# Performance work log

Measured on AMD Instinct MI355X. Metric: run time of the kernel, lower is better.

## Reference

```python
import jax, jax.numpy as jnp
import numpy as np

H, P, T = 256, 16, 4      # hidden_size, maxout_pool_size, max_dec_steps
B, M = 32, 600            # batch, document length

def _lstm_cell(x, h, c, W_ih, W_hh, b_ih, b_hh):
    g = x @ W_ih.T + b_ih + h @ W_hh.T + b_hh
    i, f, gg, o = jnp.split(g, 4, axis=1)  # torch gate order i,f,g,o
    c = jax.nn.sigmoid(f) * c + jax.nn.sigmoid(i) * jnp.tanh(gg)
    h = jax.nn.sigmoid(o) * jnp.tanh(c)
    return h, c

def _maxout(h, U, u_cat, mask_mult, W_lin, W1, b1, W2, b2, W12, b12):
    b, m, _ = U.shape
    r = jnp.tanh(jnp.concatenate([h, u_cat], axis=1) @ W_lin.T)                  # [b,H]
    m1_in = jnp.concatenate([U, jnp.broadcast_to(r[:, None, :], (b, m, H))], 2)  # [b,m,3H]
    m1 = (m1_in @ W1.T + b1).reshape(b, m, H, P).max(-1)                         # [b,m,H]
    m2 = (m1 @ W2.T + b2).reshape(b, m, H, P).max(-1)                            # [b,m,H]
    alpha = (jnp.concatenate([m1, m2], axis=2) @ W12.T + b12).max(-1)            # [b,m]
    return jax.nn.log_softmax(alpha + mask_mult, axis=1)

def _forward(U, d_mask, span, W_ih, W_hh, b_ih, b_hh,
             Ws_lin, Ws_m1, bs_m1, Ws_m2, bs_m2, Ws_m12, bs_m12,
             We_lin, We_m1, be_m1, We_m2, be_m2, We_m12, be_m12):
    b, m, _ = U.shape
    idxb = jnp.arange(b)
    mask_mult = (1.0 - d_mask.astype(U.dtype)) * -1e30
    s_i = jnp.zeros(b, jnp.int32)
    e_i = (jnp.sum(d_mask, 1) - 1).astype(jnp.int32)
    s_tgt, e_tgt = span[:, 0], span[:, 1]
    h = jnp.zeros((b, H), U.dtype)
    c = jnp.zeros((b, H), U.dtype)
    mask_s = mask_e = None
    res_s, res_e, res_ms, res_me, losses = [], [], [], [], []
    u_s = U[idxb, s_i]
    for t in range(T):
        u_e = U[idxb, e_i]
        u_cat = jnp.concatenate([u_s, u_e], axis=1)
        h, c = _lstm_cell(u_cat, h, c, W_ih, W_hh, b_ih, b_hh)
        # start pointer
        lsm = _maxout(h, U, u_cat, mask_mult, Ws_lin, Ws_m1, bs_m1, Ws_m2, bs_m2, Ws_m12, bs_m12)
        idx = jnp.argmax(lsm, axis=1).astype(jnp.int32)
        if t == 0:
            mask_s = jnp.ones(b, bool)
        else:
            idx = idx * mask_s.astype(jnp.int32)
            prev = s_i * mask_s.astype(jnp.int32)
            mask_s = idx != prev
        loss_s = jnp.mean(-jnp.take_along_axis(lsm, s_tgt[:, None], 1)[:, 0]) * mask_s.astype(U.dtype)
        s_i = idx
        u_s = U[idxb, s_i]
        # end pointer
        u_cat2 = jnp.concatenate([u_s, u_e], axis=1)
        lsm_e = _maxout(h, U, u_cat2, mask_mult, We_lin, We_m1, be_m1, We_m2, be_m2, We_m12, be_m12)
        idx_e = jnp.argmax(lsm_e, axis=1).astype(jnp.int32)
        if t == 0:
            mask_e = jnp.ones(b, bool)
        else:
            idx_e = idx_e * mask_e.astype(jnp.int32)
            prev_e = e_i * mask_e.astype(jnp.int32)
            mask_e = idx_e != prev_e
        loss_e = jnp.mean(-jnp.take_along_axis(lsm_e, e_tgt[:, None], 1)[:, 0]) * mask_e.astype(U.dtype)
        e_i = idx_e
        losses.append(loss_s + loss_e)
        res_s.append(s_i); res_ms.append(mask_s)
        res_e.append(e_i); res_me.append(mask_e)
    pos_s = jnp.sum(jnp.stack(res_ms, 1).astype(jnp.int32), 1) - 1
    p1 = jnp.take_along_axis(jnp.stack(res_s, 1), pos_s[:, None], 1)[:, 0]
    pos_e = jnp.sum(jnp.stack(res_me, 1).astype(jnp.int32), 1) - 1
    p2 = jnp.take_along_axis(jnp.stack(res_e, 1), pos_e[:, None], 1)[:, 0]
    loss = jnp.mean(jnp.sum(jnp.stack(losses, 1), 1) / T)
    return loss, p1, p2

def setup_inputs():
    key = jax.random.key(0)
    ks = jax.random.split(key, 16)
    U = jax.random.normal(ks[0], (B, M, 2 * H), jnp.float32)
    lengths = jax.random.randint(ks[1], (B,), M // 2, M + 1)
    d_mask = (jnp.arange(M)[None, :] < lengths[:, None]).astype(jnp.int32)
    span = jax.random.randint(ks[2], (B, 2), 0, M // 2).astype(jnp.int32)
    def w(k, shape, fan_in):
        return (jax.random.normal(k, shape, jnp.float32) / np.float32(np.sqrt(fan_in)))
    b_ih = jnp.zeros(4 * H, jnp.float32).at[H:2 * H].set(1.0)  # forget-gate bias init
    params = {
        'W_ih': w(ks[3], (4 * H, 4 * H), 4 * H), 'W_hh': w(ks[4], (4 * H, H), H),
        'b_ih': b_ih, 'b_hh': jnp.zeros(4 * H, jnp.float32),
        'Ws_lin': w(ks[5], (H, 5 * H), 5 * H),
        'Ws_m1': w(ks[6], (H * P, 3 * H), 3 * H), 'bs_m1': jnp.zeros(H * P, jnp.float32),
        'Ws_m2': w(ks[7], (H * P, H), H), 'bs_m2': jnp.zeros(H * P, jnp.float32),
        'Ws_m12': w(ks[8], (P, 2 * H), 2 * H), 'bs_m12': jnp.zeros(P, jnp.float32),
        'We_lin': w(ks[9], (H, 5 * H), 5 * H),
        'We_m1': w(ks[10], (H * P, 3 * H), 3 * H), 'be_m1': jnp.zeros(H * P, jnp.float32),
        'We_m2': w(ks[11], (H * P, H), H), 'be_m2': jnp.zeros(H * P, jnp.float32),
        'We_m12': w(ks[12], (P, 2 * H), 2 * H), 'be_m12': jnp.zeros(P, jnp.float32),
    }
    return {'U': U, 'd_mask': d_mask, 'span': span, **params}

def reference(U, d_mask, span, W_ih, W_hh, b_ih, b_hh,
              Ws_lin, Ws_m1, bs_m1, Ws_m2, bs_m2, Ws_m12, bs_m12,
              We_lin, We_m1, be_m1, We_m2, be_m2, We_m12, be_m12):
    return _forward(U, d_mask, span, W_ih, W_hh, b_ih, b_hh,
                    Ws_lin, Ws_m1, bs_m1, Ws_m2, bs_m2, Ws_m12, bs_m12,
                    We_lin, We_m1, be_m1, We_m2, be_m2, We_m12, be_m12)
```

## Files before the change

kernel.cpp:

```cpp
#include <hip/hip_runtime.h>
#include <math.h>

namespace {

typedef unsigned short u16;
typedef __attribute__((ext_vector_type(4))) float f32x4;
typedef __attribute__((ext_vector_type(8))) _Float16 f16x8;
typedef __attribute__((ext_vector_type(4))) _Float16 f16x4;

constexpr int B = 32;
constexpr int M = 600;
constexpr int H = 256;
constexpr int TSTEPS = 4;
constexpr int HP = 4096;
constexpr int BM = B * M;
constexpr int TWOH = 512;
constexpr int THREEH = 768;
constexpr int FOURH = 1024;
constexpr int FIVEH = 1280;
constexpr int NTILES = BM / 128;

__device__ __forceinline__ float sigf(float x) { return 1.0f / (1.0f + expf(-x)); }

__device__ __forceinline__ void gload16(const u16* g, u16* l) {
    __builtin_amdgcn_global_load_lds(
        (const __attribute__((address_space(1))) void*)g,
        (__attribute__((address_space(3))) void*)l, 16, 0, 0);
}

__global__ void k_init(const int* __restrict__ d_mask,
                       float* __restrict__ h, float* __restrict__ c,
                       float* __restrict__ loss_vec,
                       int* __restrict__ s_i, int* __restrict__ e_i,
                       int* __restrict__ p1r, int* __restrict__ p2r)
{
    int tid = threadIdx.x;
    for (int i = tid; i < B * H; i += 256) { h[i] = 0.f; c[i] = 0.f; }
    if (tid < B) {
        loss_vec[tid] = 0.f;
        s_i[tid] = 0;
        int s = 0;
        const int* row = d_mask + tid * M;
        for (int m = 0; m < M; ++m) s += row[m];
        e_i[tid] = s - 1;
        p1r[tid] = 0; p2r[tid] = 0;
    }
}

__global__ __launch_bounds__(128) void k_flags(const int* __restrict__ d_mask,
                                               int* __restrict__ flags)
{
    int bm = blockIdx.x * 128 + threadIdx.x;
    int cnt = __syncthreads_count(d_mask[bm]);
    if (threadIdx.x == 0) flags[blockIdx.x] = (cnt == 0) ? 1 : 0;
}

__global__ __launch_bounds__(256) void k_gather(
    const float* __restrict__ U, const int* __restrict__ s_i,
    const int* __restrict__ e_i, float* __restrict__ u_cat)
{
    int idx = blockIdx.x * 256 + threadIdx.x;
    int b = idx >> 9, k = idx & 511;
    u_cat[b * FOURH + k]       = U[((size_t)b * M + s_i[b]) * TWOH + k];
    u_cat[b * FOURH + 512 + k] = U[((size_t)b * M + e_i[b]) * TWOH + k];
}

__global__ __launch_bounds__(256) void k_lstm_gemm2(
    const float* __restrict__ U, const int* __restrict__ s_i,
    const int* __restrict__ e_i, const float* __restrict__ h,
    const float* __restrict__ W_ih, const float* __restrict__ W_hh,
    const float* __restrict__ b_ih, const float* __restrict__ b_hh,
    float* __restrict__ g)
{
    int idx = blockIdx.x * 256 + threadIdx.x;
    int b = idx >> 10, j = idx & 1023;
    const float* us = U + ((size_t)b * M + s_i[b]) * TWOH;
    const float* ue = U + ((size_t)b * M + e_i[b]) * TWOH;
    float acc = 0.f;
    const float4* x4 = (const float4*)us;
    const float4* wi4 = (const float4*)(W_ih + (size_t)j * FOURH);
    #pragma unroll 4
    for (int k = 0; k < TWOH / 4; ++k) {
        float4 a = x4[k], w = wi4[k];
        acc += a.x * w.x + a.y * w.y + a.z * w.z + a.w * w.w;
    }
    const float4* y4 = (const float4*)ue;
    const float4* wi4b = wi4 + TWOH / 4;
    #pragma unroll 4
    for (int k = 0; k < TWOH / 4; ++k) {
        float4 a = y4[k], w = wi4b[k];
        acc += a.x * w.x + a.y * w.y + a.z * w.z + a.w * w.w;
    }
    const float4* h4 = (const float4*)(h + b * H);
    const float4* wh4 = (const float4*)(W_hh + (size_t)j * H);
    #pragma unroll 4
    for (int k = 0; k < H / 4; ++k) {
        float4 a = h4[k], w = wh4[k];
        acc += a.x * w.x + a.y * w.y + a.z * w.z + a.w * w.w;
    }
    g[idx] = acc + b_ih[j] + b_hh[j];
}

__global__ __launch_bounds__(256) void k_lstm_gemm(
    const float* __restrict__ u_cat, const float* __restrict__ h,
    const float* __restrict__ W_ih, const float* __restrict__ W_hh,
    const float* __restrict__ b_ih, const float* __restrict__ b_hh,
    float* __restrict__ g)
{
    int idx = blockIdx.x * 256 + threadIdx.x;
    int b = idx >> 10, j = idx & 1023;
    float acc = 0.f;
    const float4* x4 = (const float4*)(u_cat + b * FOURH);
    const float4* wi4 = (const float4*)(W_ih + (size_t)j * FOURH);
    #pragma unroll 4
    for (int k = 0; k < FOURH / 4; ++k) {
        float4 a = x4[k], w = wi4[k];
        acc += a.x * w.x + a.y * w.y + a.z * w.z + a.w * w.w;
    }
    const float4* h4 = (const float4*)(h + b * H);
    const float4* wh4 = (const float4*)(W_hh + (size_t)j * H);
    #pragma unroll 4
    for (int k = 0; k < H / 4; ++k) {
        float4 a = h4[k], w = wh4[k];
        acc += a.x * w.x + a.y * w.y + a.z * w.z + a.w * w.w;
    }
    g[idx] = acc + b_ih[j] + b_hh[j];
}

__global__ __launch_bounds__(256) void k_lstm_gates(
    const float* __restrict__ g, float* __restrict__ h, float* __restrict__ c)
{
    int idx = blockIdx.x * 256 + threadIdx.x;
    int b = idx >> 8, i = idx & (H - 1);
    const float* gr = g + b * FOURH;
    float gi = gr[i], gf = gr[H + i], gg = gr[2 * H + i], go = gr[3 * H + i];
    float cn = sigf(gf) * c[idx] + sigf(gi) * tanhf(gg);
    c[idx] = cn;
    h[idx] = sigf(go) * tanhf(cn);
}

__global__ __launch_bounds__(256) void k_r2(
    const float* __restrict__ h, const float* __restrict__ U,
    const int* __restrict__ s_i, const int* __restrict__ e_i,
    const float* __restrict__ W_lin, float* __restrict__ r)
{
    int gid = blockIdx.x * 256 + threadIdx.x;
    int out = gid >> 2;
    int part = gid & 3;
    int b = out >> 8, i = out & (H - 1);
    const float4* w4 = (const float4*)(W_lin + (size_t)i * FIVEH);
    const float4* h4 = (const float4*)(h + b * H);
    const float4* us4 = (const float4*)(U + ((size_t)b * M + s_i[b]) * TWOH);
    const float4* ue4 = (const float4*)(U + ((size_t)b * M + e_i[b]) * TWOH);
    float acc = 0.f;
    int k0 = part * 80;
    #pragma unroll 4
    for (int kk = k0; kk < k0 + 80; ++kk) {
        float4 a;
        if (kk < 64) a = h4[kk];
        else if (kk < 192) a = us4[kk - 64];
        else a = ue4[kk - 192];
        float4 ww = w4[kk];
        acc += a.x * ww.x + a.y * ww.y + a.z * ww.z + a.w * ww.w;
    }
    acc += __shfl_xor(acc, 1);
    acc += __shfl_xor(acc, 2);
    if (part == 0) r[out] = tanhf(acc);
}

__global__ __launch_bounds__(256) void k_r(
    const float* __restrict__ h, const float* __restrict__ u_cat,
    const float* __restrict__ W_lin, float* __restrict__ r)
{
    int idx = blockIdx.x * 256 + threadIdx.x;
    int b = idx >> 8, i = idx & (H - 1);
    const float* w = W_lin + (size_t)i * FIVEH;
    float acc = 0.f;
    const float4* h4 = (const float4*)(h + b * H);
    const float4* w4 = (const float4*)w;
    #pragma unroll 4
    for (int k = 0; k < H / 4; ++k) {
        float4 a = h4[k], ww = w4[k];
        acc += a.x * ww.x + a.y * ww.y + a.z * ww.z + a.w * ww.w;
    }
    const float4* x4 = (const float4*)(u_cat + b * FOURH);
    const float4* w4b = (const float4*)(w + H);
    #pragma unroll 4
    for (int k = 0; k < FOURH / 4; ++k) {
        float4 a = x4[k], ww = w4b[k];
        acc += a.x * ww.x + a.y * ww.y + a.z * ww.z + a.w * ww.w;
    }
    r[idx] = tanhf(acc);
}

__global__ __launch_bounds__(256) void k_rW(
    const float* __restrict__ r, const float* __restrict__ W1,
    const float* __restrict__ b1, float* __restrict__ rW)
{
    int idx = blockIdx.x * 256 + threadIdx.x;
    int b = idx >> 12, j = idx & (HP - 1);
    const float4* r4 = (const float4*)(r + b * H);
    const float4* w4 = (const float4*)(W1 + (size_t)j * THREEH + TWOH);
    float acc = 0.f;
    #pragma unroll 4
    for (int k = 0; k < H / 4; ++k) {
        float4 a = r4[k], w = w4[k];
        acc += a.x * w.x + a.y * w.y + a.z * w.z + a.w * w.w;
    }
    rW[idx] = acc + b1[j];
}

__global__ __launch_bounds__(256) void k_rW2(
    const float* __restrict__ r, const float* __restrict__ Wt,
    const float* __restrict__ b1, float* __restrict__ rW)
{
    const int b = blockIdx.y;
    const int j = blockIdx.x * 256 + threadIdx.x;
    __shared__ float sr[256];
    sr[threadIdx.x] = r[b * H + threadIdx.x];
    __syncthreads();
    float acc = b1[j];
    #pragma unroll 4
    for (int k = 0; k < H; ++k) acc += sr[k] * Wt[(size_t)k * HP + j];
    rW[(size_t)b * HP + j] = acc;
}

__global__ __launch_bounds__(256) void k_transp2(
    const float* __restrict__ W, float* __restrict__ Wt)
{
    __shared__ float s[32][33];
    int j0 = (blockIdx.x & 127) << 5;
    int k0 = (blockIdx.x >> 7) << 5;
    int tx = threadIdx.x & 31, ty = threadIdx.x >> 5;
    #pragma unroll
    for (int kk = 0; kk < 4; ++kk) {
        int jl = ty + kk * 8;
        s[jl][tx] = W[(size_t)(j0 + jl) * THREEH + TWOH + k0 + tx];
    }
    __syncthreads();
    #pragma unroll
    for (int kk = 0; kk < 4; ++kk) {
        int kl = ty + kk * 8;
        Wt[(size_t)(k0 + kl) * HP + j0 + tx] = s[tx][kl];
    }
}

__global__ __launch_bounds__(256) void k_cvtH(
    const float* __restrict__ src, int ld, int Kc, _Float16* __restrict__ dst)
{
    int i4 = blockIdx.x * 256 + threadIdx.x;
    int perrow = Kc >> 2;
    int row = i4 / perrow;
    int kc = (i4 - row * perrow) << 2;
    float4 v = *(const float4*)(src + (size_t)row * ld + kc);
    f16x4 o;
    o[0] = (_Float16)v.x; o[1] = (_Float16)v.y; o[2] = (_Float16)v.z; o[3] = (_Float16)v.w;
    *(f16x4*)(dst + (size_t)row * Kc + kc) = o;
}

template <int EPI>
__global__ __launch_bounds__(256, 4) void gemmJ(
    const _Float16* __restrict__ A, const _Float16* __restrict__ Bw,
    int K, const float* __restrict__ extra, const int* __restrict__ skip,
    float* __restrict__ Cf, _Float16* __restrict__ Ch)
{
    if (skip[blockIdx.y]) return;
    __shared__ __align__(16) u16 sA[2][128 * 32];
    __shared__ __align__(16) u16 sB[2][128 * 32];
    const int tid = threadIdx.x;
    const int w = tid >> 6, lane = tid & 63;
    const int row0 = blockIdx.y * 128, col0 = blockIdx.x * 128;
    const int wm = w & 1, wn = w >> 1;

    const int r1g = tid >> 2,        k1 = (tid & 3) ^ ((r1g >> 1) & 3);
    const int r2g = (tid + 256) >> 2, k2 = ((tid + 256) & 3) ^ ((r2g >> 1) & 3);
    const size_t gA1 = (size_t)(row0 + r1g) * K + k1 * 8;
    const size_t gA2 = (size_t)(row0 + r2g) * K + k2 * 8;
    const size_t gB1 = (size_t)(col0 + r1g) * K + k1 * 8;
    const size_t gB2 = (size_t)(col0 + r2g) * K + k2 * 8;

    f32x4 acc[4][4] = {};

    gload16((const u16*)(A  + gA1), &sA[0][tid * 8]);
    gload16((const u16*)(A  + gA2), &sA[0][(tid + 256) * 8]);
    gload16((const u16*)(Bw + gB1), &sB[0][tid * 8]);
    gload16((const u16*)(Bw + gB2), &sB[0][(tid + 256) * 8]);

    const int iters = K >> 5;
    const int mrow = lane & 15;
    const int kg = lane >> 4;
    const int slot = kg ^ ((mrow >> 1) & 3);
    const int eoff = slot << 3;

    for (int it = 0; it < iters; ++it) {
        const int cur = it & 1;
        __syncthreads();
        if (it + 1 < iters) {
            const int k0n = (it + 1) << 5;
            gload16((const u16*)(A  + gA1 + k0n), &sA[1 - cur][tid * 8]);
            gload16((const u16*)(A  + gA2 + k0n), &sA[1 - cur][(tid + 256) * 8]);
            gload16((const u16*)(Bw + gB1 + k0n), &sB[1 - cur][tid * 8]);
            gload16((const u16*)(Bw + gB2 + k0n), &sB[1 - cur][(tid + 256) * 8]);
        }
        const u16* pa = &sA[cur][(wm * 64 + mrow) * 32 + eoff];
        const u16* pb = &sB[cur][(wn * 64 + mrow) * 32 + eoff];
        f16x8 fa[4], fb[4];
        #pragma unroll
        for (int f = 0; f < 4; ++f) {
            fa[f] = *(const f16x8*)(pa + f * 16 * 32);
            fb[f] = *(const f16x8*)(pb + f * 16 * 32);
        }
        #pragma unroll
        for (int i = 0; i < 4; ++i) {
            #pragma unroll
            for (int j = 0; j < 4; ++j) {
                acc[i][j] = __builtin_amdgcn_mfma_f32_16x16x32_f16(fa[i], fb[j], acc[i][j], 0, 0, 0);
            }
        }
    }

    const int cq = lane & 15, rq = lane >> 4;
    if (EPI == 4) {
        #pragma unroll
        for (int i = 0; i < 4; ++i) {
            #pragma unroll
            for (int j = 0; j < 4; ++j) {
                int col = col0 + wn * 64 + j * 16 + cq;
                #pragma unroll
                for (int rr = 0; rr < 4; ++rr) {
                    int row = row0 + wm * 64 + i * 16 + rq * 4 + rr;
                    Ch[(size_t)row * HP + col] = (_Float16)acc[i][j][rr];
                }
            }
        }
    } else if (EPI == 1) {
        #pragma unroll
        for (int j = 0; j < 4; ++j) {
            int col = col0 + wn * 64 + j * 16 + cq;
            int gcol = (col0 >> 4) + wn * 4 + j;
            float bv = extra[col];
            #pragma unroll
            for (int i = 0; i < 4; ++i) {
                #pragma unroll
                for (int rr = 0; rr < 4; ++rr) {
                    float v = acc[i][j][rr] + bv;
                    v = fmaxf(v, __shfl_xor(v, 1));
                    v = fmaxf(v, __shfl_xor(v, 2));
                    v = fmaxf(v, __shfl_xor(v, 4));
                    v = fmaxf(v, __shfl_xor(v, 8));
                    if (cq == 0) {
                        int row = row0 + wm * 64 + i * 16 + rq * 4 + rr;
                        Ch[(size_t)row * H + gcol] = (_Float16)v;
                    }
                }
            }
        }
    } else {
        const int rbase = row0 + wm * 64;
        const int b0 = rbase / M;
        const int bnd = (b0 + 1) * M;
        #pragma unroll
        for (int j = 0; j < 4; ++j) {
            int col = col0 + wn * 64 + j * 16 + cq;
            int gcol = (col0 >> 4) + wn * 4 + j;
            float e0 = extra[(size_t)b0 * HP + col];
            float e1 = extra[(size_t)(b0 + 1) * HP + col];
            #pragma unroll
            for (int i = 0; i < 4; ++i) {
                #pragma unroll
                for (int rr = 0; rr < 4; ++rr) {
                    int row = rbase + i * 16 + rq * 4 + rr;
                    float v = acc[i][j][rr] + ((row >= bnd) ? e1 : e0);
                    v = fmaxf(v, __shfl_xor(v, 1));
                    v = fmaxf(v, __shfl_xor(v, 2));
                    v = fmaxf(v, __shfl_xor(v, 4));
                    v = fmaxf(v, __shfl_xor(v, 8));
                    if (cq == 0)
                        Ch[(size_t)row * H + gcol] = (_Float16)v;
                }
            }
        }
    }
}

__global__ __launch_bounds__(256) void k_m1A16(
    const _Float16* __restrict__ A, const float* __restrict__ rW,
    _Float16* __restrict__ m1)
{
    int idx = blockIdx.x * 256 + threadIdx.x;
    int bm = idx >> 8;
    int h = idx & (H - 1);
    int b = bm / M;
    const f16x8* a8 = (const f16x8*)(A + (size_t)bm * HP + (h << 4));
    const float4* r4 = (const float4*)(rW + (size_t)b * HP + (h << 4));
    f16x8 a0 = a8[0], a1 = a8[1];
    float4 ra = r4[0], rb = r4[1], rc = r4[2], rd = r4[3];
    float mx;
    mx = fmaxf(fmaxf(fmaxf((float)a0[0] + ra.x, (float)a0[1] + ra.y),
                     fmaxf((float)a0[2] + ra.z, (float)a0[3] + ra.w)),
         fmaxf(fmaxf((float)a0[4] + rb.x, (float)a0[5] + rb.y),
               fmaxf((float)a0[6] + rb.z, (float)a0[7] + rb.w)));
    mx = fmaxf(mx,
         fmaxf(fmaxf(fmaxf((float)a1[0] + rc.x, (float)a1[1] + rc.y),
                     fmaxf((float)a1[2] + rc.z, (float)a1[3] + rc.w)),
               fmaxf(fmaxf((float)a1[4] + rd.x, (float)a1[5] + rd.y),
                     fmaxf((float)a1[6] + rd.z, (float)a1[7] + rd.w))));
    m1[idx] = (_Float16)mx;
}

template <int EPI>
__global__ __launch_bounds__(256) void gemm64(
    const float* __restrict__ Ag, int lda,
    const float* __restrict__ Bg, int ldb,
    const float* __restrict__ extra,
    float* __restrict__ C, int K, int ldc)
{
    __shared__ float As[16][68];
    __shared__ float Bs[16][68];
    const int tid = threadIdx.x;
    const int tx = tid & 15;
    const int ty = tid >> 4;
    const int row0 = blockIdx.y * 64;
    const int col0 = blockIdx.x * 64;
    const int lr = tid >> 2;
    const int lk = (tid & 3) << 2;
    const float* Aload = Ag + (size_t)(row0 + lr) * lda + lk;
    const float* Bload = Bg + (size_t)(col0 + lr) * ldb + lk;
    float acc[4][4] = {};
    for (int k0 = 0; k0 < K; k0 += 16) {
        float4 av = *(const float4*)(Aload + k0);
        float4 bv = *(const float4*)(Bload + k0);
        __syncthreads();
        As[lk + 0][lr] = av.x; As[lk + 1][lr] = av.y; As[lk + 2][lr] = av.z; As[lk + 3][lr] = av.w;
        Bs[lk + 0][lr] = bv.x; Bs[lk + 1][lr] = bv.y; Bs[lk + 2][lr] = bv.z; Bs[lk + 3][lr] = bv.w;
        __syncthreads();
        #pragma unroll
        for (int k = 0; k < 16; ++k) {
            float4 a4 = *(const float4*)(&As[k][ty << 2]);
            float4 b4 = *(const float4*)(&Bs[k][tx << 2]);
            acc[0][0] += a4.x * b4.x; acc[0][1] += a4.x * b4.y; acc[0][2] += a4.x * b4.z; acc[0][3] += a4.x * b4.w;
            acc[1][0] += a4.y * b4.x; acc[1][1] += a4.y * b4.y; acc[1][2] += a4.y * b4.z; acc[1][3] += a4.y * b4.w;
            acc[2][0] += a4.z * b4.x; acc[2][1] += a4.z * b4.y; acc[2][2] += a4.z * b4.z; acc[2][3] += a4.z * b4.w;
            acc[3][0] += a4.w * b4.x; acc[3][1] += a4.w * b4.y; acc[3][2] += a4.w * b4.z; acc[3][3] += a4.w * b4.w;
        }
    }
    if (EPI == 1) {
        const int cb = col0 + (tx << 2);
        float b0 = extra[cb], b1v = extra[cb + 1], b2v = extra[cb + 2], b3v = extra[cb + 3];
        #pragma unroll
        for (int i = 0; i < 4; ++i) {
            float mth = fmaxf(fmaxf(acc[i][0] + b0, acc[i][1] + b1v),
                              fmaxf(acc[i][2] + b2v, acc[i][3] + b3v));
            float r1 = fmaxf(mth, __shfl_xor(mth, 1));
            float r2 = fmaxf(r1, __shfl_xor(r1, 2));
            if ((tx & 3) == 0)
                C[(size_t)(row0 + (ty << 2) + i) * ldc + (col0 >> 4) + (tx >> 2)] = r2;
        }
    } else if (EPI == 2) {
        const int cb = col0 + (tx << 2);
        #pragma unroll
        for (int i = 0; i < 4; ++i) {
            int row = row0 + (ty << 2) + i;
            int b = row / M;
            const float* rw = extra + (size_t)b * HP + cb;
            float mth = fmaxf(fmaxf(acc[i][0] + rw[0], acc[i][1] + rw[1]),
                              fmaxf(acc[i][2] + rw[2], acc[i][3] + rw[3]));
            float r1 = fmaxf(mth, __shfl_xor(mth, 1));
            float r2 = fmaxf(r1, __shfl_xor(r1, 2));
            if ((tx & 3) == 0)
                C[(size_t)row * ldc + (col0 >> 4) + (tx >> 2)] = r2;
        }
    }
}

__global__ __launch_bounds__(256) void k_alpha(
    const float* __restrict__ m1, const float* __restrict__ m2,
    const float* __restrict__ W12, const float* __restrict__ b12,
    const int* __restrict__ d_mask, float* __restrict__ alpha)
{
    __shared__ float Ws[16 * 512];
    const int tid = threadIdx.x;
    for (int i = tid; i < 16 * 512; i += 256) Ws[i] = W12[i];
    __syncthreads();
    const int wave = tid >> 6, lane = tid & 63;
    const int bm = blockIdx.x * 4 + wave;
    const float* r1 = m1 + (size_t)bm * H;
    const float* r2 = m2 + (size_t)bm * H;
    float acc[16] = {};
    #pragma unroll
    for (int q = 0; q < 4; ++q) {
        int k = lane + (q << 6);
        float x = r1[k];
        #pragma unroll
        for (int p = 0; p < 16; ++p) acc[p] += x * Ws[p * 512 + k];
    }
    #pragma unroll
    for (int q = 0; q < 4; ++q) {
        int k = lane + (q << 6);
        float x = r2[k];
        #pragma unroll
        for (int p = 0; p < 16; ++p) acc[p] += x * Ws[p * 512 + 256 + k];
    }
    #pragma unroll
    for (int p = 0; p < 16; ++p) {
        float v = acc[p];
        v += __shfl_xor(v, 1);  v += __shfl_xor(v, 2);  v += __shfl_xor(v, 4);
        v += __shfl_xor(v, 8);  v += __shfl_xor(v, 16); v += __shfl_xor(v, 32);
        acc[p] = v;
    }
    if (lane == 0) {
        float mx = -INFINITY;
        #pragma unroll
        for (int p = 0; p < 16; ++p) mx = fmaxf(mx, acc[p] + b12[p]);
        alpha[bm] = d_mask[bm] ? mx : -1e30f;
    }
}

__global__ __launch_bounds__(256) void k_alpha2(
    const _Float16* __restrict__ m1, const _Float16* __restrict__ m2,
    const float* __restrict__ W12, const float* __restrict__ b12,
    const int* __restrict__ d_mask, float* __restrict__ alpha)
{
    __shared__ float Ws[16 * 512];
    const int tid = threadIdx.x;
    for (int i = tid; i < 16 * 512; i += 256) Ws[i] = W12[i];
    __syncthreads();
    const int wave = tid >> 6, lane = tid & 63;
    const int bm0 = blockIdx.x * 16 + wave * 4;
    for (int rr = 0; rr < 4; ++rr) {
        const int bm = bm0 + rr;
        if (!d_mask[bm]) {
            if (lane == 0) alpha[bm] = -1e30f;
            continue;
        }
        const _Float16* r1 = m1 + (size_t)bm * H;
        const _Float16* r2 = m2 + (size_t)bm * H;
        float acc[16] = {};
        #pragma unroll
        for (int q = 0; q < 4; ++q) {
            int k = lane + (q << 6);
            float x = (float)r1[k];
            #pragma unroll
            for (int p = 0; p < 16; ++p) acc[p] += x * Ws[p * 512 + k];
        }
        #pragma unroll
        for (int q = 0; q < 4; ++q) {
            int k = lane + (q << 6);
            float x = (float)r2[k];
            #pragma unroll
            for (int p = 0; p < 16; ++p) acc[p] += x * Ws[p * 512 + 256 + k];
        }
        #pragma unroll
        for (int p = 0; p < 16; ++p) {
            float v = acc[p];
            v += __shfl_xor(v, 1);  v += __shfl_xor(v, 2);  v += __shfl_xor(v, 4);
            v += __shfl_xor(v, 8);  v += __shfl_xor(v, 16); v += __shfl_xor(v, 32);
            acc[p] = v;
        }
        if (lane == 0) {
            float mx = -INFINITY;
            #pragma unroll
            for (int p = 0; p < 16; ++p) mx = fmaxf(mx, acc[p] + b12[p]);
            alpha[bm] = mx;
        }
    }
}

__global__ __launch_bounds__(1024) void k_smu(
    const float* __restrict__ alpha, const int* __restrict__ span, int phase,
    int* __restrict__ pos, int* __restrict__ mask,
    int* __restrict__ prun, float* __restrict__ loss_vec, int t)
{
    __shared__ float s_loss[B];
    __shared__ int s_idx[B];
    const int wave = threadIdx.x >> 6, lane = threadIdx.x & 63;
    for (int b = wave; b < B; b += 16) {
        const float* row = alpha + b * M;
        float best = -INFINITY; int bidx = 0;
        for (int m = lane; m < M; m += 64) {
            float v = row[m];
            if (v > best) { best = v; bidx = m; }
        }
        #pragma unroll
        for (int off = 1; off < 64; off <<= 1) {
            float v2 = __shfl_xor(best, off);
            int i2 = __shfl_xor(bidx, off);
            if (v2 > best || (v2 == best && i2 < bidx)) { best = v2; bidx = i2; }
        }
        float ps = 0.f;
        for (int m = lane; m < M; m += 64) ps += expf(row[m] - best);
        #pragma unroll
        for (int off = 32; off > 0; off >>= 1) ps += __shfl_xor(ps, off);
        if (lane == 0) {
            float lse = best + logf(ps);
            int tgt = span[b * 2 + phase];
            s_loss[b] = -(row[tgt] - lse);
            s_idx[b] = bidx;
        }
    }
    __syncthreads();
    if (wave == 0) {
        int b = lane;
        int active = (b < B) ? 1 : 0;
        int ni = 0, nm = 0;
        if (active) {
            int id = s_idx[b];
            if (t == 0) { nm = 1; ni = id; }
            else {
                int om = mask[b];
                ni = id * om;
                int prev = pos[b] * om;
                nm = (ni != prev) ? 1 : 0;
            }
        }
        float v = active ? s_loss[b] : 0.f;
        #pragma unroll
        for (int off = 32; off > 0; off >>= 1) v += __shfl_xor(v, off);
        float S = v * (1.0f / (float)B);
        if (active) {
            pos[b] = ni;
            mask[b] = nm;
            if (nm) { prun[b] = ni; loss_vec[b] += S; }
        }
    }
}

__global__ __launch_bounds__(256) void k_softmax(
    const float* __restrict__ alpha, const int* __restrict__ span, int phase,
    float* __restrict__ loss_term, int* __restrict__ idx_out)
{
    __shared__ float sv[256];
    __shared__ int si[256];
    const int b = blockIdx.x, tid = threadIdx.x;
    const float* row = alpha + b * M;
    float best = -INFINITY; int bidx = 0;
    for (int m = tid; m < M; m += 256) {
        float v = row[m];
        if (v > best) { best = v; bidx = m; }
    }
    sv[tid] = best; si[tid] = bidx;
    __syncthreads();
    for (int s = 128; s > 0; s >>= 1) {
        if (tid < s) {
            float v2 = sv[tid + s]; int i2 = si[tid + s];
            if (v2 > sv[tid] || (v2 == sv[tid] && i2 < si[tid])) { sv[tid] = v2; si[tid] = i2; }
        }
        __syncthreads();
    }
    float bmax = sv[0]; int amax = si[0];
    __syncthreads();
    float ps = 0.f;
    for (int m = tid; m < M; m += 256) ps += expf(row[m] - bmax);
    sv[tid] = ps;
    __syncthreads();
    for (int s = 128; s > 0; s >>= 1) {
        if (tid < s) sv[tid] += sv[tid + s];
        __syncthreads();
    }
    if (tid == 0) {
        float lse = bmax + logf(sv[0]);
        int tgt = span[b * 2 + phase];
        loss_term[b] = -(row[tgt] - lse);
        idx_out[b] = amax;
    }
}

__global__ void k_update(const int* __restrict__ idx_in, const float* __restrict__ loss_term,
                         int* __restrict__ pos, int* __restrict__ mask,
                         int* __restrict__ prun, float* __restrict__ loss_vec, int t)
{
    int b = threadIdx.x;
    int active = (b < B) ? 1 : 0;
    int ni = 0, nm = 0;
    if (active) {
        int id = idx_in[b];
        if (t == 0) { nm = 1; ni = id; }
        else {
            int om = mask[b];
            ni = id * om;
            int prev = pos[b] * om;
            nm = (ni != prev) ? 1 : 0;
        }
    }
    float v = active ? loss_term[b] : 0.f;
    #pragma unroll
    for (int off = 32; off > 0; off >>= 1) v += __shfl_xor(v, off);
    float S = v * (1.0f / (float)B);
    if (active) {
        pos[b] = ni;
        mask[b] = nm;
        if (nm) { prun[b] = ni; loss_vec[b] += S; }
    }
}

__global__ void k_finalize(const float* __restrict__ loss_vec, const int* __restrict__ p1r,
                           const int* __restrict__ p2r, float* __restrict__ out)
{
    int b = threadIdx.x;
    float v = (b < B) ? loss_vec[b] : 0.f;
    #pragma unroll
    for (int off = 32; off > 0; off >>= 1) v += __shfl_xor(v, off);
    if (b == 0) out[0] = v / (float)(B * TSTEPS);
    if (b < B) {
        out[1 + b] = (float)p1r[b];
        out[1 + B + b] = (float)p2r[b];
    }
}

}

extern "C" void kernel_launch(void* const* d_in, const int* in_sizes, int n_in,
                              void* d_out, int out_size, void* d_ws, size_t ws_size,
                              hipStream_t stream)
{
    const float* U      = (const float*)d_in[0];
    const int*   d_mask = (const int*)d_in[1];
    const int*   span   = (const int*)d_in[2];
    const float* W_ih   = (const float*)d_in[3];
    const float* W_hh   = (const float*)d_in[4];
    const float* b_ih   = (const float*)d_in[5];
    const float* b_hh   = (const float*)d_in[6];
    const float* Ws_lin = (const float*)d_in[7];
    const float* Ws_m1  = (const float*)d_in[8];
    const float* bs_m1  = (const float*)d_in[9];
    const float* Ws_m2  = (const float*)d_in[10];
    const float* bs_m2  = (const float*)d_in[11];
    const float* Ws_m12 = (const float*)d_in[12];
    const float* bs_m12 = (const float*)d_in[13];
    const float* We_lin = (const float*)d_in[14];
    const float* We_m1  = (const float*)d_in[15];
    const float* be_m1  = (const float*)d_in[16];
    const float* We_m2  = (const float*)d_in[17];
    const float* be_m2  = (const float*)d_in[18];
    const float* We_m12 = (const float*)d_in[19];
    const float* be_m12 = (const float*)d_in[20];

    float* ws = (float*)d_ws;
    size_t o = 0;
    float* m2b   = ws + o; o += (size_t)BM * H;
    float* alphab= ws + o; o += BM;
    float* u_cat = ws + o; o += B * FOURH;
    float* gbuf  = ws + o; o += B * FOURH;
    float* hbuf  = ws + o; o += B * H;
    float* cbuf  = ws + o; o += B * H;
    float* rbuf  = ws + o; o += B * H;
    float* rWb   = ws + o; o += B * HP;
    float* loss_term = ws + o; o += B;
    float* loss_vec  = ws + o; o += B;
    int* ib = (int*)(ws + o); o += 8 * B + 160;
    int* idxb   = ib + 0 * B;
    int* s_i    = ib + 1 * B;
    int* e_i    = ib + 2 * B;
    int* mask_s = ib + 3 * B;
    int* mask_e = ib + 4 * B;
    int* p1r    = ib + 5 * B;
    int* p2r    = ib + 6 * B;
    int* flags  = ib + 8 * B;
    size_t o_common = (o + 3) & ~(size_t)3;

    float* m1b = ws + o_common;

    size_t p = o_common;
    float* Wt_s = ws + p; p += (size_t)H * HP;
    float* Wt_e = ws + p; p += (size_t)H * HP;
    _Float16* hs = (_Float16*)(ws + p);
    size_t q = 0;
    _Float16* Uh  = hs + q; q += (size_t)BM * TWOH;
    _Float16* W1s = hs + q; q += (size_t)HP * TWOH;
    _Float16* W1e = hs + q; q += (size_t)HP * TWOH;
    _Float16* W2s = hs + q; q += (size_t)HP * H;
    _Float16* W2e = hs + q; q += (size_t)HP * H;
    _Float16* m1b16 = hs + q; q += (size_t)BM * H;
    q = (q + 7) & ~(size_t)7;
    const size_t need2 = p * sizeof(float) + q * sizeof(_Float16);
    _Float16* A_s16 = hs + q;
    _Float16* A_e16 = A_s16 + (size_t)BM * HP;
    const size_t need15s = need2 + (size_t)BM * HP * sizeof(_Float16);
    const size_t need16  = need15s + (size_t)BM * HP * sizeof(_Float16);

    _Float16* m2h = (_Float16*)m2b;

    const int tier = (ws_size >= need16) ? 16
                   : (ws_size >= need15s) ? 15
                   : (ws_size >= need2) ? 2 : 3;

    k_init<<<1, 256, 0, stream>>>(d_mask, hbuf, cbuf, loss_vec, s_i, e_i, p1r, p2r);

    if (tier != 3) {
        k_flags<<<NTILES, 128, 0, stream>>>(d_mask, flags);
        k_cvtH<<<BM * TWOH / 4 / 256, 256, 0, stream>>>(U, TWOH, TWOH, Uh);
        k_cvtH<<<HP * TWOH / 4 / 256, 256, 0, stream>>>(Ws_m1, THREEH, TWOH, W1s);
        k_cvtH<<<HP * TWOH / 4 / 256, 256, 0, stream>>>(We_m1, THREEH, TWOH, W1e);
        k_cvtH<<<HP * H / 4 / 256, 256, 0, stream>>>(Ws_m2, H, H, W2s);
        k_cvtH<<<HP * H / 4 / 256, 256, 0, stream>>>(We_m2, H, H, W2e);
        k_transp2<<<1024, 256, 0, stream>>>(Ws_m1, Wt_s);
        k_transp2<<<1024, 256, 0, stream>>>(We_m1, Wt_e);

        dim3 gJ(HP / 128, NTILES);
        if (tier >= 15) {
            gemmJ<4><<<gJ, 256, 0, stream>>>(Uh, W1s, TWOH, nullptr, flags, nullptr, A_s16);
        }
        if (tier == 16) {
            gemmJ<4><<<gJ, 256, 0, stream>>>(Uh, W1e, TWOH, nullptr, flags, nullptr, A_e16);
        }

        for (int t = 0; t < TSTEPS; ++t) {
            k_lstm_gemm2<<<128, 256, 0, stream>>>(U, s_i, e_i, hbuf, W_ih, W_hh, b_ih, b_hh, gbuf);
            k_lstm_gates<<<32, 256, 0, stream>>>(gbuf, hbuf, cbuf);

            k_r2<<<128, 256, 0, stream>>>(hbuf, U, s_i, e_i, Ws_lin, rbuf);
            k_rW2<<<dim3(HP / 256, B), 256, 0, stream>>>(rbuf, Wt_s, bs_m1, rWb);
            if (tier >= 15)
                k_m1A16<<<BM * H / 256, 256, 0, stream>>>(A_s16, rWb, m1b16);
            else
                gemmJ<3><<<gJ, 256, 0, stream>>>(Uh, W1s, TWOH, rWb, flags, nullptr, m1b16);
            gemmJ<1><<<gJ, 256, 0, stream>>>(m1b16, W2s, H, bs_m2, flags, nullptr, m2h);
            k_alpha2<<<BM / 16, 256, 0, stream>>>(m1b16, m2h, Ws_m12, bs_m12, d_mask, alphab);
            k_smu<<<1, 1024, 0, stream>>>(alphab, span, 0, s_i, mask_s, p1r, loss_vec, t);

            k_r2<<<128, 256, 0, stream>>>(hbuf, U, s_i, e_i, We_lin, rbuf);
            k_rW2<<<dim3(HP / 256, B), 256, 0, stream>>>(rbuf, Wt_e, be_m1, rWb);
            if (tier == 16)
                k_m1A16<<<BM * H / 256, 256, 0, stream>>>(A_e16, rWb, m1b16);
            else
                gemmJ<3><<<gJ, 256, 0, stream>>>(Uh, W1e, TWOH, rWb, flags, nullptr, m1b16);
            gemmJ<1><<<gJ, 256, 0, stream>>>(m1b16, W2e, H, be_m2, flags, nullptr, m2h);
            k_alpha2<<<BM / 16, 256, 0, stream>>>(m1b16, m2h, We_m12, be_m12, d_mask, alphab);
            k_smu<<<1, 1024, 0, stream>>>(alphab, span, 1, e_i, mask_e, p2r, loss_vec, t);
        }
    } else {
        dim3 gemm_grid(HP / 64, BM / 64);
        for (int t = 0; t < TSTEPS; ++t) {
            k_gather<<<64, 256, 0, stream>>>(U, s_i, e_i, u_cat);
            k_lstm_gemm<<<128, 256, 0, stream>>>(u_cat, hbuf, W_ih, W_hh, b_ih, b_hh, gbuf);
            k_lstm_gates<<<32, 256, 0, stream>>>(gbuf, hbuf, cbuf);

            k_r<<<32, 256, 0, stream>>>(hbuf, u_cat, Ws_lin, rbuf);
            k_rW<<<512, 256, 0, stream>>>(rbuf, Ws_m1, bs_m1, rWb);
            gemm64<2><<<gemm_grid, 256, 0, stream>>>(U, TWOH, Ws_m1, THREEH, rWb, m1b, TWOH, H);
            gemm64<1><<<gemm_grid, 256, 0, stream>>>(m1b, H, Ws_m2, H, bs_m2, m2b, H, H);
            k_alpha<<<BM / 4, 256, 0, stream>>>(m1b, m2b, Ws_m12, bs_m12, d_mask, alphab);
            k_softmax<<<B, 256, 0, stream>>>(alphab, span, 0, loss_term, idxb);
            k_update<<<1, 64, 0, stream>>>(idxb, loss_term, s_i, mask_s, p1r, loss_vec, t);

            k_gather<<<64, 256, 0, stream>>>(U, s_i, e_i, u_cat);

            k_r<<<32, 256, 0, stream>>>(hbuf, u_cat, We_lin, rbuf);
            k_rW<<<512, 256, 0, stream>>>(rbuf, We_m1, be_m1, rWb);
            gemm64<2><<<gemm_grid, 256, 0, stream>>>(U, TWOH, We_m1, THREEH, rWb, m1b, TWOH, H);
            gemm64<1><<<gemm_grid, 256, 0, stream>>>(m1b, H, We_m2, H, be_m2, m2b, H, H);
            k_alpha<<<BM / 4, 256, 0, stream>>>(m1b, m2b, We_m12, be_m12, d_mask, alphab);
            k_softmax<<<B, 256, 0, stream>>>(alphab, span, 1, loss_term, idxb);
            k_update<<<1, 64, 0, stream>>>(idxb, loss_term, e_i, mask_e, p2r, loss_vec, t);
        }
    }

    k_finalize<<<1, 64, 0, stream>>>(loss_vec, p1r, p2r, (float*)d_out);
}
```

Baseline: 2.511 ms.

## Use MFMA for alpha projection and fp16 transposed weights for rW

Replaces the scalar shared-memory alpha kernel with one that uses 16x16x32 fp16 MFMA over 16-row tiles, with the W12 weights converted to fp16 once up front. The transposed W1 slice used for the rW matvec is now stored in fp16 and read two columns per thread, halving its memory traffic. These changes cut the per-step cost of alpha and rW, at the price of fp16 rounding of W12 and W1, which could flip argmax ties. Workspace layout also shifts to drop the fp32 transposed buffers.

```diff
diff --git a/kernel.cpp b/kernel.cpp
--- a/kernel.cpp
+++ b/kernel.cpp
@@ -7,6 +7,7 @@
 typedef __attribute__((ext_vector_type(4))) float f32x4;
 typedef __attribute__((ext_vector_type(8))) _Float16 f16x8;
 typedef __attribute__((ext_vector_type(4))) _Float16 f16x4;
+typedef __attribute__((ext_vector_type(2))) _Float16 f16x2;
 
 constexpr int B = 32;
 constexpr int M = 600;
@@ -210,23 +211,29 @@
     rW[idx] = acc + b1[j];
 }
 
-__global__ __launch_bounds__(256) void k_rW2(
-    const float* __restrict__ r, const float* __restrict__ Wt,
+__global__ __launch_bounds__(256) void k_rW2h(
+    const float* __restrict__ r, const _Float16* __restrict__ Wt,
     const float* __restrict__ b1, float* __restrict__ rW)
 {
     const int b = blockIdx.y;
-    const int j = blockIdx.x * 256 + threadIdx.x;
+    const int j = (blockIdx.x * 256 + threadIdx.x) * 2;
     __shared__ float sr[256];
     sr[threadIdx.x] = r[b * H + threadIdx.x];
     __syncthreads();
-    float acc = b1[j];
-    #pragma unroll 4
-    for (int k = 0; k < H; ++k) acc += sr[k] * Wt[(size_t)k * HP + j];
-    rW[(size_t)b * HP + j] = acc;
+    float a0 = b1[j], a1 = b1[j + 1];
+    #pragma unroll 4
+    for (int k = 0; k < H; ++k) {
+        f16x2 wv = *(const f16x2*)(Wt + (size_t)k * HP + j);
+        float x = sr[k];
+        a0 += x * (float)wv[0];
+        a1 += x * (float)wv[1];
+    }
+    rW[(size_t)b * HP + j]     = a0;
+    rW[(size_t)b * HP + j + 1] = a1;
 }
 
 __global__ __launch_bounds__(256) void k_transp2(
-    const float* __restrict__ W, float* __restrict__ Wt)
+    const float* __restrict__ W, _Float16* __restrict__ Wt)
 {
     __shared__ float s[32][33];
     int j0 = (blockIdx.x & 127) << 5;
@@ -241,7 +248,7 @@
     #pragma unroll
     for (int kk = 0; kk < 4; ++kk) {
         int kl = ty + kk * 8;
-        Wt[(size_t)(k0 + kl) * HP + j0 + tx] = s[tx][kl];
+        Wt[(size_t)(k0 + kl) * HP + j0 + tx] = (_Float16)s[tx][kl];
     }
 }
 
@@ -516,52 +523,43 @@
     }
 }
 
-__global__ __launch_bounds__(256) void k_alpha2(
+__global__ __launch_bounds__(256) void k_alphaM(
     const _Float16* __restrict__ m1, const _Float16* __restrict__ m2,
-    const float* __restrict__ W12, const float* __restrict__ b12,
+    const _Float16* __restrict__ W12h, const float* __restrict__ b12,
     const int* __restrict__ d_mask, float* __restrict__ alpha)
 {
-    __shared__ float Ws[16 * 512];
-    const int tid = threadIdx.x;
-    for (int i = tid; i < 16 * 512; i += 256) Ws[i] = W12[i];
-    __syncthreads();
-    const int wave = tid >> 6, lane = tid & 63;
-    const int bm0 = blockIdx.x * 16 + wave * 4;
-    for (int rr = 0; rr < 4; ++rr) {
-        const int bm = bm0 + rr;
-        if (!d_mask[bm]) {
-            if (lane == 0) alpha[bm] = -1e30f;
-            continue;
-        }
-        const _Float16* r1 = m1 + (size_t)bm * H;
-        const _Float16* r2 = m2 + (size_t)bm * H;
-        float acc[16] = {};
-        #pragma unroll
-        for (int q = 0; q < 4; ++q) {
-            int k = lane + (q << 6);
-            float x = (float)r1[k];
-            #pragma unroll
-            for (int p = 0; p < 16; ++p) acc[p] += x * Ws[p * 512 + k];
-        }
-        #pragma unroll
-        for (int q = 0; q < 4; ++q) {
-            int k = lane + (q << 6);
-            float x = (float)r2[k];
-            #pragma unroll
-            for (int p = 0; p < 16; ++p) acc[p] += x * Ws[p * 512 + 256 + k];
-        }
-        #pragma unroll
-        for (int p = 0; p < 16; ++p) {
-            float v = acc[p];
-            v += __shfl_xor(v, 1);  v += __shfl_xor(v, 2);  v += __shfl_xor(v, 4);
-            v += __shfl_xor(v, 8);  v += __shfl_xor(v, 16); v += __shfl_xor(v, 32);
-            acc[p] = v;
-        }
-        if (lane == 0) {
-            float mx = -INFINITY;
-            #pragma unroll
-            for (int p = 0; p < 16; ++p) mx = fmaxf(mx, acc[p] + b12[p]);
-            alpha[bm] = mx;
+    const int wave = threadIdx.x >> 6, lane = threadIdx.x & 63;
+    const int bm0 = blockIdx.x * 64 + wave * 16;
+    const int rsel = lane & 15, kg = lane >> 4;
+    f16x8 fb[16];
+    #pragma unroll
+    for (int kb = 0; kb < 16; ++kb)
+        fb[kb] = *(const f16x8*)(W12h + (size_t)rsel * 512 + kb * 32 + kg * 8);
+    f32x4 acc = {};
+    const _Float16* r1 = m1 + (size_t)(bm0 + rsel) * H + kg * 8;
+    const _Float16* r2 = m2 + (size_t)(bm0 + rsel) * H + kg * 8;
+    #pragma unroll
+    for (int kb = 0; kb < 8; ++kb) {
+        f16x8 fa = *(const f16x8*)(r1 + kb * 32);
+        acc = __builtin_amdgcn_mfma_f32_16x16x32_f16(fa, fb[kb], acc, 0, 0, 0);
+    }
+    #pragma unroll
+    for (int kb = 0; kb < 8; ++kb) {
+        f16x8 fa = *(const f16x8*)(r2 + kb * 32);
+        acc = __builtin_amdgcn_mfma_f32_16x16x32_f16(fa, fb[8 + kb], acc, 0, 0, 0);
+    }
+    const int cq = lane & 15, rq = lane >> 4;
+    float bv = b12[cq];
+    #pragma unroll
+    for (int reg = 0; reg < 4; ++reg) {
+        float v = acc[reg] + bv;
+        v = fmaxf(v, __shfl_xor(v, 1));
+        v = fmaxf(v, __shfl_xor(v, 2));
+        v = fmaxf(v, __shfl_xor(v, 4));
+        v = fmaxf(v, __shfl_xor(v, 8));
+        if (cq == 0) {
+            int bm = bm0 + rq * 4 + reg;
+            alpha[bm] = d_mask[bm] ? v : -1e30f;
         }
     }
 }
@@ -760,19 +758,20 @@
 
     float* m1b = ws + o_common;
 
-    size_t p = o_common;
-    float* Wt_s = ws + p; p += (size_t)H * HP;
-    float* Wt_e = ws + p; p += (size_t)H * HP;
-    _Float16* hs = (_Float16*)(ws + p);
+    _Float16* hs = (_Float16*)(ws + o_common);
     size_t q = 0;
-    _Float16* Uh  = hs + q; q += (size_t)BM * TWOH;
-    _Float16* W1s = hs + q; q += (size_t)HP * TWOH;
-    _Float16* W1e = hs + q; q += (size_t)HP * TWOH;
-    _Float16* W2s = hs + q; q += (size_t)HP * H;
-    _Float16* W2e = hs + q; q += (size_t)HP * H;
+    _Float16* Uh    = hs + q; q += (size_t)BM * TWOH;
+    _Float16* W1s   = hs + q; q += (size_t)HP * TWOH;
+    _Float16* W1e   = hs + q; q += (size_t)HP * TWOH;
+    _Float16* W2s   = hs + q; q += (size_t)HP * H;
+    _Float16* W2e   = hs + q; q += (size_t)HP * H;
     _Float16* m1b16 = hs + q; q += (size_t)BM * H;
+    _Float16* Wth_s = hs + q; q += (size_t)H * HP;
+    _Float16* Wth_e = hs + q; q += (size_t)H * HP;
+    _Float16* W12sh = hs + q; q += 16 * 512;
+    _Float16* W12eh = hs + q; q += 16 * 512;
     q = (q + 7) & ~(size_t)7;
-    const size_t need2 = p * sizeof(float) + q * sizeof(_Float16);
+    const size_t need2 = o_common * sizeof(float) + q * sizeof(_Float16);
     _Float16* A_s16 = hs + q;
     _Float16* A_e16 = A_s16 + (size_t)BM * HP;
     const size_t need15s = need2 + (size_t)BM * HP * sizeof(_Float16);
@@ -793,8 +792,10 @@
         k_cvtH<<<HP * TWOH / 4 / 256, 256, 0, stream>>>(We_m1, THREEH, TWOH, W1e);
         k_cvtH<<<HP * H / 4 / 256, 256, 0, stream>>>(Ws_m2, H, H, W2s);
         k_cvtH<<<HP * H / 4 / 256, 256, 0, stream>>>(We_m2, H, H, W2e);
-        k_transp2<<<1024, 256, 0, stream>>>(Ws_m1, Wt_s);
-        k_transp2<<<1024, 256, 0, stream>>>(We_m1, Wt_e);
+        k_cvtH<<<16 * 512 / 4 / 256, 256, 0, stream>>>(Ws_m12, 512, 512, W12sh);
+        k_cvtH<<<16 * 512 / 4 / 256, 256, 0, stream>>>(We_m12, 512, 512, W12eh);
+        k_transp2<<<1024, 256, 0, stream>>>(Ws_m1, Wth_s);
+        k_transp2<<<1024, 256, 0, stream>>>(We_m1, Wth_e);
 
         dim3 gJ(HP / 128, NTILES);
         if (tier >= 15) {
@@ -809,23 +810,23 @@
             k_lstm_gates<<<32, 256, 0, stream>>>(gbuf, hbuf, cbuf);
 
             k_r2<<<128, 256, 0, stream>>>(hbuf, U, s_i, e_i, Ws_lin, rbuf);
-            k_rW2<<<dim3(HP / 256, B), 256, 0, stream>>>(rbuf, Wt_s, bs_m1, rWb);
+            k_rW2h<<<dim3(HP / 512, B), 256, 0, stream>>>(rbuf, Wth_s, bs_m1, rWb);
             if (tier >= 15)
                 k_m1A16<<<BM * H / 256, 256, 0, stream>>>(A_s16, rWb, m1b16);
             else
                 gemmJ<3><<<gJ, 256, 0, stream>>>(Uh, W1s, TWOH, rWb, flags, nullptr, m1b16);
             gemmJ<1><<<gJ, 256, 0, stream>>>(m1b16, W2s, H, bs_m2, flags, nullptr, m2h);
-            k_alpha2<<<BM / 16, 256, 0, stream>>>(m1b16, m2h, Ws_m12, bs_m12, d_mask, alphab);
+            k_alphaM<<<BM / 64, 256, 0, stream>>>(m1b16, m2h, W12sh, bs_m12, d_mask, alphab);
             k_smu<<<1, 1024, 0, stream>>>(alphab, span, 0, s_i, mask_s, p1r, loss_vec, t);
 
             k_r2<<<128, 256, 0, stream>>>(hbuf, U, s_i, e_i, We_lin, rbuf);
-            k_rW2<<<dim3(HP / 256, B), 256, 0, stream>>>(rbuf, Wt_e, be_m1, rWb);
+            k_rW2h<<<dim3(HP / 512, B), 256, 0, stream>>>(rbuf, Wth_e, be_m1, rWb);
             if (tier == 16)
                 k_m1A16<<<BM * H / 256, 256, 0, stream>>>(A_e16, rWb, m1b16);
             else
                 gemmJ<3><<<gJ, 256, 0, stream>>>(Uh, W1e, TWOH, rWb, flags, nullptr, m1b16);
             gemmJ<1><<<gJ, 256, 0, stream>>>(m1b16, W2e, H, be_m2, flags, nullptr, m2h);
-            k_alpha2<<<BM / 16, 256, 0, stream>>>(m1b16, m2h, We_m12, be_m12, d_mask, alphab);
+            k_alphaM<<<BM / 64, 256, 0, stream>>>(m1b16, m2h, W12eh, be_m12, d_mask, alphab);
             k_smu<<<1, 1024, 0, stream>>>(alphab, span, 1, e_i, mask_e, p2r, loss_vec, t);
         }
     } else {
```

Result: faster. 2.414 ms (-3.9%).
